# Kernel optimization log

Measured on AMD Instinct MI355X. Metric: run time of the kernel, lower is better.

Reference implementation:

```python
import jax, jax.numpy as jnp
import numpy as np

N_NODES = 100000
N_EDGES = 3200000
IN_DIM = 512
LATENT_DIM = 128


def spmm(row, col, vals, z, n):
    # sparse [n,n] @ z: out[r] = sum_e vals[e] * z[col[e]] for edges with row[e]==r
    msgs = vals[:, None] * z[col]  # [E, d]
    return jax.ops.segment_sum(msgs, row, num_segments=n)


def setup_inputs() -> dict:
    key = jax.random.key(0)
    k1, k2, k3, k4, k5, k6, k7 = jax.random.split(key, 7)
    x = jax.random.normal(k1, (N_NODES, IN_DIM), dtype=jnp.float32)
    # xavier-uniform-like init
    lim_e = float(np.sqrt(6.0 / (IN_DIM + LATENT_DIM)))
    W_enc = jax.random.uniform(k2, (IN_DIM, LATENT_DIM), minval=-lim_e, maxval=lim_e, dtype=jnp.float32)
    W_dec = jax.random.uniform(k3, (LATENT_DIM, IN_DIM), minval=-lim_e, maxval=lim_e, dtype=jnp.float32)
    row = jax.random.randint(k4, (N_EDGES,), 0, N_NODES, dtype=jnp.int32)
    col = jax.random.randint(k5, (N_EDGES,), 0, N_NODES, dtype=jnp.int32)
    vals = jax.random.uniform(k6, (N_EDGES,), dtype=jnp.float32)
    perm = jax.random.permutation(k7, N_NODES).astype(jnp.int32)
    return {"x": x, "W_enc": W_enc, "W_dec": W_dec, "vals": vals,
            "row": row, "col": col, "perm": perm}


def reference(x, W_enc, W_dec, vals, row, col, perm):
    n = x.shape[0]
    # encoder GCN: h = adj @ (x @ W_enc)
    h = spmm(row, col, vals, x @ W_enc, n)
    # decoder GCN: out = adj @ (h @ W_dec)
    out = spmm(row, col, vals, h @ W_dec, n)
    # corrupted view: row-permuted features through the encoder
    x_a = x[perm]
    h_a = spmm(row, col, vals, x_a @ W_enc, n)
    return (out, h, h_a)
```

## Files before the change

kernel.cpp:

```cpp
#include <hip/hip_runtime.h>
#include <hip/hip_bf16.h>


#define THREADS 256


__global__ void zero_i32(int* __restrict__ p, int n) {
    int i = blockIdx.x * blockDim.x + threadIdx.x;
    if (i < n) p[i] = 0;
}

__global__ void copy_i32(const int* __restrict__ src, int* __restrict__ dst, int n) {
    int i = blockIdx.x * blockDim.x + threadIdx.x;
    if (i < n) dst[i] = src[i];
}

__global__ void hist_rows(const int* __restrict__ row, int* __restrict__ cnt, int E) {
    for (int e = blockIdx.x * blockDim.x + threadIdx.x; e < E; e += gridDim.x * blockDim.x)
        atomicAdd(&cnt[row[e]], 1);
}

__global__ void scan_partial(const int* __restrict__ cnt, int* __restrict__ bsum, int n) {
    __shared__ int red[256];
    int t = threadIdx.x;
    int base = blockIdx.x * 1024 + t * 4;
    int s = 0;
#pragma unroll
    for (int i = 0; i < 4; ++i) {
        int idx = base + i;
        if (idx < n) s += cnt[idx];
    }
    red[t] = s;
    __syncthreads();
    for (int off = 128; off > 0; off >>= 1) {
        if (t < off) red[t] += red[t + off];
        __syncthreads();
    }
    if (t == 0) bsum[blockIdx.x] = red[0];
}

__global__ void scan_bsum(const int* __restrict__ bsum, int* __restrict__ bscan,
                          int nb, int* __restrict__ rowptr, int n, int E) {
    __shared__ int s[128];
    int t = threadIdx.x;
    int v = (t < nb) ? bsum[t] : 0;
    s[t] = v;
    __syncthreads();
    for (int off = 1; off < 128; off <<= 1) {
        int x = (t >= off) ? s[t - off] : 0;
        __syncthreads();
        s[t] += x;
        __syncthreads();
    }
    if (t < nb) bscan[t] = s[t] - v;
    if (t == 0) rowptr[n] = E;
}

__global__ void scan_final(const int* __restrict__ cnt, const int* __restrict__ bscan,
                           int* __restrict__ rowptr, int n) {
    __shared__ int tsum[256];
    int t = threadIdx.x;
    int base = blockIdx.x * 1024 + t * 4;
    int v[4];
#pragma unroll
    for (int i = 0; i < 4; ++i) {
        int idx = base + i;
        v[i] = (idx < n) ? cnt[idx] : 0;
    }
    int tot = v[0] + v[1] + v[2] + v[3];
    tsum[t] = tot;
    __syncthreads();
    for (int off = 1; off < 256; off <<= 1) {
        int x = (t >= off) ? tsum[t - off] : 0;
        __syncthreads();
        tsum[t] += x;
        __syncthreads();
    }
    int run = tsum[t] - tot + bscan[blockIdx.x];
#pragma unroll
    for (int i = 0; i < 4; ++i) {
        int idx = base + i;
        if (idx < n) rowptr[idx] = run;
        run += v[i];
    }
}

__global__ void scatter_edges(const int* __restrict__ row, const int* __restrict__ col,
                              const float* __restrict__ vals, int* __restrict__ cursor,
                              int* __restrict__ scol, float* __restrict__ sval, int E) {
    for (int e = blockIdx.x * blockDim.x + threadIdx.x; e < E; e += gridDim.x * blockDim.x) {
        int r = row[e];
        int p = atomicAdd(&cursor[r], 1);
        scol[p] = col[e];
        sval[p] = vals[e];
    }
}

__global__ __launch_bounds__(256) void gemm_f32(const float* __restrict__ A,
                                                const float* __restrict__ B,
                                                float* __restrict__ C,
                                                int M, int N, int K) {
    __shared__ float As[16][68];
    __shared__ float Bs[16][128];
    int t = threadIdx.x;
    int tr = t >> 5;
    int tc = t & 31;
    int rbase = blockIdx.x * 64;
    int cb = blockIdx.y * 128;

    float acc[8][4];
#pragma unroll
    for (int i = 0; i < 8; ++i)
#pragma unroll
        for (int j = 0; j < 4; ++j) acc[i][j] = 0.f;

    int arow = t >> 2;
    int akq = (t & 3) * 4;

    for (int kt = 0; kt < K; kt += 16) {
        float4 av = make_float4(0.f, 0.f, 0.f, 0.f);
        if (rbase + arow < M)
            av = *(const float4*)&A[(size_t)(rbase + arow) * K + kt + akq];
        As[akq + 0][arow] = av.x;
        As[akq + 1][arow] = av.y;
        As[akq + 2][arow] = av.z;
        As[akq + 3][arow] = av.w;
        {
            int s0 = t;
            int k0 = s0 >> 5, c0 = (s0 & 31) * 4;
            *(float4*)&Bs[k0][c0] = *(const float4*)&B[(size_t)(kt + k0) * N + cb + c0];
            int s1 = t + 256;
            int k1 = s1 >> 5, c1 = (s1 & 31) * 4;
            *(float4*)&Bs[k1][c1] = *(const float4*)&B[(size_t)(kt + k1) * N + cb + c1];
        }
        __syncthreads();
#pragma unroll
        for (int kk = 0; kk < 16; ++kk) {
            float4 a0 = *(const float4*)&As[kk][tr * 8];
            float4 a1 = *(const float4*)&As[kk][tr * 8 + 4];
            float4 b = *(const float4*)&Bs[kk][tc * 4];
            float a[8] = {a0.x, a0.y, a0.z, a0.w, a1.x, a1.y, a1.z, a1.w};
#pragma unroll
            for (int i = 0; i < 8; ++i) {
                acc[i][0] += a[i] * b.x;
                acc[i][1] += a[i] * b.y;
                acc[i][2] += a[i] * b.z;
                acc[i][3] += a[i] * b.w;
            }
        }
        __syncthreads();
    }
#pragma unroll
    for (int i = 0; i < 8; ++i) {
        int r = rbase + tr * 8 + i;
        if (r < M)
            *(float4*)&C[(size_t)r * N + cb + tc * 4] =
                make_float4(acc[i][0], acc[i][1], acc[i][2], acc[i][3]);
    }
}

__global__ __launch_bounds__(256) void spmm128(const int* __restrict__ rowptr,
                                               const int* __restrict__ scol,
                                               const float* __restrict__ sval,
                                               const float* __restrict__ z,
                                               float* __restrict__ out,
                                               const int* __restrict__ perm, int n) {
    int t = threadIdx.x;
    int r = blockIdx.x * 8 + (t >> 5);
    if (r >= n) return;
    int lane4 = (t & 31) * 4;
    int s = rowptr[r], e1 = rowptr[r + 1];
    float4 acc = make_float4(0.f, 0.f, 0.f, 0.f);
    for (int e = s; e < e1; ++e) {
        int c = scol[e];
        if (perm) c = perm[c];
        float v = sval[e];
        float4 zv = *(const float4*)&z[(size_t)c * 128 + lane4];
        acc.x += v * zv.x;
        acc.y += v * zv.y;
        acc.z += v * zv.z;
        acc.w += v * zv.w;
    }
    *(float4*)&out[(size_t)r * 128 + lane4] = acc;
}


extern "C" void kernel_launch(void* const* d_in, const int* in_sizes, int n_in,
                              void* d_out, int out_size, void* d_ws, size_t ws_size,
                              hipStream_t stream) {
    const float* x     = (const float*)d_in[0];
    const float* W_enc = (const float*)d_in[1];
    const float* W_dec = (const float*)d_in[2];
    const float* vals  = (const float*)d_in[3];
    const int*   row   = (const int*)d_in[4];
    const int*   col   = (const int*)d_in[5];
    const int*   perm  = (const int*)d_in[6];
    const int n = in_sizes[6];
    const int E = in_sizes[4];
    const int IN = 512, L = 128;

    float* out0  = (float*)d_out;
    float* outh  = out0 + (size_t)n * IN;
    float* outha = outh + (size_t)n * L;

    char* w = (char*)d_ws;
    auto alloc = [&](size_t bytes) -> char* {
        char* p = w;
        w += (bytes + 255) & ~(size_t)255;
        return p;
    };
    float* z1     = (float*)alloc((size_t)n * L * 4);
    float* g      = (float*)alloc((size_t)n * L * 4);
    int*   scol   = (int*)alloc((size_t)E * 4);
    float* sval   = (float*)alloc((size_t)E * 4);
    int*   rowptr = (int*)alloc((size_t)(n + 1) * 4);
    int*   cursor = (int*)alloc((size_t)n * 4);
    int*   cnt    = (int*)alloc((size_t)n * 4);
    int*   bsum   = (int*)alloc(128 * 4);
    int*   bscan  = (int*)alloc(128 * 4);

    const int nb = (n + 1023) / 1024;

    hipLaunchKernelGGL(zero_i32, dim3((n + 255) / 256), dim3(256), 0, stream, cnt, n);
    hipLaunchKernelGGL(hist_rows, dim3(2048), dim3(256), 0, stream, row, cnt, E);
    hipLaunchKernelGGL(scan_partial, dim3(nb), dim3(256), 0, stream, cnt, bsum, n);
    hipLaunchKernelGGL(scan_bsum, dim3(1), dim3(128), 0, stream, bsum, bscan, nb, rowptr, n, E);
    hipLaunchKernelGGL(scan_final, dim3(nb), dim3(256), 0, stream, cnt, bscan, rowptr, n);
    hipLaunchKernelGGL(copy_i32, dim3((n + 255) / 256), dim3(256), 0, stream, rowptr, cursor, n);
    hipLaunchKernelGGL(scatter_edges, dim3(2048), dim3(256), 0, stream,
                       row, col, vals, cursor, scol, sval, E);

    hipLaunchKernelGGL(gemm_f32, dim3((n + 63) / 64, 1), dim3(256), 0, stream,
                       x, W_enc, z1, n, L, IN);
    hipLaunchKernelGGL(spmm128, dim3((n + 7) / 8), dim3(256), 0, stream,
                       rowptr, scol, sval, z1, outh, (const int*)nullptr, n);
    hipLaunchKernelGGL(spmm128, dim3((n + 7) / 8), dim3(256), 0, stream,
                       rowptr, scol, sval, z1, outha, perm, n);
    hipLaunchKernelGGL(spmm128, dim3((n + 7) / 8), dim3(256), 0, stream,
                       rowptr, scol, sval, outh, g, (const int*)nullptr, n);
    hipLaunchKernelGGL(gemm_f32, dim3((n + 63) / 64, 4), dim3(256), 0, stream,
                       g, W_dec, out0, n, IN, L);
}
```

Measured before the change: 1.767 ms.

## Store SpMM operands in bf16, pack edges, fuse encoder and corrupted SpMMs

The encoder GEMM now writes z in bf16, and h is also stored as a bf16 copy for the decoder SpMM. This halves the bytes of the random gathers that dominate the SpMM kernels. Column and value are packed into one 8-byte edge record, and the h and h_a SpMMs are fused so each edge is read once with two gathers. Each row is handled by 16 lanes with 8 features per lane. The cost is bf16 rounding error in the intermediates, which may exceed the output tolerance.

Result: faster. 1.460 ms (-17.4%).

```diff
diff --git a/kernel.cpp b/kernel.cpp
--- a/kernel.cpp
+++ b/kernel.cpp
@@ -2,7 +2,15 @@
 #include <hip/hip_bf16.h>
 
 
-#define THREADS 256
+typedef unsigned int uint;
+typedef unsigned short ushort;
+
+__device__ inline ushort f2bf(float f) {
+    uint u = __float_as_uint(f);
+    return (ushort)((u + 0x7FFFu + ((u >> 16) & 1u)) >> 16);
+}
+__device__ inline float bflo(uint u) { return __uint_as_float(u << 16); }
+__device__ inline float bfhi(uint u) { return __uint_as_float(u & 0xFFFF0000u); }
 
 
 __global__ void zero_i32(int* __restrict__ p, int n) {
@@ -87,18 +95,18 @@
 
 __global__ void scatter_edges(const int* __restrict__ row, const int* __restrict__ col,
                               const float* __restrict__ vals, int* __restrict__ cursor,
-                              int* __restrict__ scol, float* __restrict__ sval, int E) {
+                              uint2* __restrict__ ep, int E) {
     for (int e = blockIdx.x * blockDim.x + threadIdx.x; e < E; e += gridDim.x * blockDim.x) {
         int r = row[e];
         int p = atomicAdd(&cursor[r], 1);
-        scol[p] = col[e];
-        sval[p] = vals[e];
+        ep[p] = make_uint2((uint)col[e], __float_as_uint(vals[e]));
     }
 }
 
 __global__ __launch_bounds__(256) void gemm_f32(const float* __restrict__ A,
                                                 const float* __restrict__ B,
-                                                float* __restrict__ C,
+                                                float* __restrict__ Cf,
+                                                ushort* __restrict__ Cb,
                                                 int M, int N, int K) {
     __shared__ float As[16][68];
     __shared__ float Bs[16][128];
@@ -153,35 +161,88 @@
 #pragma unroll
     for (int i = 0; i < 8; ++i) {
         int r = rbase + tr * 8 + i;
-        if (r < M)
-            *(float4*)&C[(size_t)r * N + cb + tc * 4] =
-                make_float4(acc[i][0], acc[i][1], acc[i][2], acc[i][3]);
-    }
-}
-
-__global__ __launch_bounds__(256) void spmm128(const int* __restrict__ rowptr,
-                                               const int* __restrict__ scol,
-                                               const float* __restrict__ sval,
-                                               const float* __restrict__ z,
-                                               float* __restrict__ out,
-                                               const int* __restrict__ perm, int n) {
-    int t = threadIdx.x;
-    int r = blockIdx.x * 8 + (t >> 5);
+        if (r < M) {
+            if (Cb) {
+                ushort4 o;
+                o.x = f2bf(acc[i][0]);
+                o.y = f2bf(acc[i][1]);
+                o.z = f2bf(acc[i][2]);
+                o.w = f2bf(acc[i][3]);
+                *(ushort4*)&Cb[(size_t)r * N + cb + tc * 4] = o;
+            } else {
+                *(float4*)&Cf[(size_t)r * N + cb + tc * 4] =
+                    make_float4(acc[i][0], acc[i][1], acc[i][2], acc[i][3]);
+            }
+        }
+    }
+}
+
+__global__ __launch_bounds__(256) void spmm_fused(const int* __restrict__ rowptr,
+                                                  const uint2* __restrict__ ep,
+                                                  const ushort* __restrict__ zb,
+                                                  const int* __restrict__ perm,
+                                                  float* __restrict__ outh,
+                                                  float* __restrict__ outha,
+                                                  ushort* __restrict__ hb, int n) {
+    int t = threadIdx.x;
+    int r = blockIdx.x * 16 + (t >> 4);
     if (r >= n) return;
-    int lane4 = (t & 31) * 4;
+    int lo = (t & 15) * 8;
     int s = rowptr[r], e1 = rowptr[r + 1];
-    float4 acc = make_float4(0.f, 0.f, 0.f, 0.f);
+    float ah[8] = {0, 0, 0, 0, 0, 0, 0, 0};
+    float aa[8] = {0, 0, 0, 0, 0, 0, 0, 0};
     for (int e = s; e < e1; ++e) {
-        int c = scol[e];
-        if (perm) c = perm[c];
-        float v = sval[e];
-        float4 zv = *(const float4*)&z[(size_t)c * 128 + lane4];
-        acc.x += v * zv.x;
-        acc.y += v * zv.y;
-        acc.z += v * zv.z;
-        acc.w += v * zv.w;
-    }
-    *(float4*)&out[(size_t)r * 128 + lane4] = acc;
+        uint2 ed = ep[e];
+        int c = (int)ed.x;
+        float v = __uint_as_float(ed.y);
+        int c2 = perm[c];
+        uint4 za = *(const uint4*)&zb[(size_t)c * 128 + lo];
+        uint4 zp = *(const uint4*)&zb[(size_t)c2 * 128 + lo];
+        ah[0] += v * bflo(za.x); ah[1] += v * bfhi(za.x);
+        ah[2] += v * bflo(za.y); ah[3] += v * bfhi(za.y);
+        ah[4] += v * bflo(za.z); ah[5] += v * bfhi(za.z);
+        ah[6] += v * bflo(za.w); ah[7] += v * bfhi(za.w);
+        aa[0] += v * bflo(zp.x); aa[1] += v * bfhi(zp.x);
+        aa[2] += v * bflo(zp.y); aa[3] += v * bfhi(zp.y);
+        aa[4] += v * bflo(zp.z); aa[5] += v * bfhi(zp.z);
+        aa[6] += v * bflo(zp.w); aa[7] += v * bfhi(zp.w);
+    }
+    size_t o = (size_t)r * 128 + lo;
+    *(float4*)&outh[o]     = make_float4(ah[0], ah[1], ah[2], ah[3]);
+    *(float4*)&outh[o + 4] = make_float4(ah[4], ah[5], ah[6], ah[7]);
+    *(float4*)&outha[o]     = make_float4(aa[0], aa[1], aa[2], aa[3]);
+    *(float4*)&outha[o + 4] = make_float4(aa[4], aa[5], aa[6], aa[7]);
+    uint4 hp;
+    hp.x = (uint)f2bf(ah[0]) | ((uint)f2bf(ah[1]) << 16);
+    hp.y = (uint)f2bf(ah[2]) | ((uint)f2bf(ah[3]) << 16);
+    hp.z = (uint)f2bf(ah[4]) | ((uint)f2bf(ah[5]) << 16);
+    hp.w = (uint)f2bf(ah[6]) | ((uint)f2bf(ah[7]) << 16);
+    *(uint4*)&hb[o] = hp;
+}
+
+__global__ __launch_bounds__(256) void spmm_single(const int* __restrict__ rowptr,
+                                                   const uint2* __restrict__ ep,
+                                                   const ushort* __restrict__ zb,
+                                                   float* __restrict__ out, int n) {
+    int t = threadIdx.x;
+    int r = blockIdx.x * 16 + (t >> 4);
+    if (r >= n) return;
+    int lo = (t & 15) * 8;
+    int s = rowptr[r], e1 = rowptr[r + 1];
+    float ah[8] = {0, 0, 0, 0, 0, 0, 0, 0};
+    for (int e = s; e < e1; ++e) {
+        uint2 ed = ep[e];
+        int c = (int)ed.x;
+        float v = __uint_as_float(ed.y);
+        uint4 za = *(const uint4*)&zb[(size_t)c * 128 + lo];
+        ah[0] += v * bflo(za.x); ah[1] += v * bfhi(za.x);
+        ah[2] += v * bflo(za.y); ah[3] += v * bfhi(za.y);
+        ah[4] += v * bflo(za.z); ah[5] += v * bfhi(za.z);
+        ah[6] += v * bflo(za.w); ah[7] += v * bfhi(za.w);
+    }
+    size_t o = (size_t)r * 128 + lo;
+    *(float4*)&out[o]     = make_float4(ah[0], ah[1], ah[2], ah[3]);
+    *(float4*)&out[o + 4] = make_float4(ah[4], ah[5], ah[6], ah[7]);
 }
 
 
@@ -209,10 +270,10 @@
         w += (bytes + 255) & ~(size_t)255;
         return p;
     };
-    float* z1     = (float*)alloc((size_t)n * L * 4);
-    float* g      = (float*)alloc((size_t)n * L * 4);
-    int*   scol   = (int*)alloc((size_t)E * 4);
-    float* sval   = (float*)alloc((size_t)E * 4);
+    ushort* z1b   = (ushort*)alloc((size_t)n * L * 2);
+    ushort* hb    = (ushort*)alloc((size_t)n * L * 2);
+    float*  g     = (float*)alloc((size_t)n * L * 4);
+    uint2*  ep    = (uint2*)alloc((size_t)E * 8);
     int*   rowptr = (int*)alloc((size_t)(n + 1) * 4);
     int*   cursor = (int*)alloc((size_t)n * 4);
     int*   cnt    = (int*)alloc((size_t)n * 4);
@@ -228,16 +289,14 @@
     hipLaunchKernelGGL(scan_final, dim3(nb), dim3(256), 0, stream, cnt, bscan, rowptr, n);
     hipLaunchKernelGGL(copy_i32, dim3((n + 255) / 256), dim3(256), 0, stream, rowptr, cursor, n);
     hipLaunchKernelGGL(scatter_edges, dim3(2048), dim3(256), 0, stream,
-                       row, col, vals, cursor, scol, sval, E);
+                       row, col, vals, cursor, ep, E);
 
     hipLaunchKernelGGL(gemm_f32, dim3((n + 63) / 64, 1), dim3(256), 0, stream,
-                       x, W_enc, z1, n, L, IN);
-    hipLaunchKernelGGL(spmm128, dim3((n + 7) / 8), dim3(256), 0, stream,
-                       rowptr, scol, sval, z1, outh, (const int*)nullptr, n);
-    hipLaunchKernelGGL(spmm128, dim3((n + 7) / 8), dim3(256), 0, stream,
-                       rowptr, scol, sval, z1, outha, perm, n);
-    hipLaunchKernelGGL(spmm128, dim3((n + 7) / 8), dim3(256), 0, stream,
-                       rowptr, scol, sval, outh, g, (const int*)nullptr, n);
+                       x, W_enc, (float*)nullptr, z1b, n, L, IN);
+    hipLaunchKernelGGL(spmm_fused, dim3((n + 15) / 16), dim3(256), 0, stream,
+                       rowptr, ep, z1b, perm, outh, outha, hb, n);
+    hipLaunchKernelGGL(spmm_single, dim3((n + 15) / 16), dim3(256), 0, stream,
+                       rowptr, ep, hb, g, n);
     hipLaunchKernelGGL(gemm_f32, dim3((n + 63) / 64, 4), dim3(256), 0, stream,
-                       g, W_dec, out0, n, IN, L);
-}
+                       g, W_dec, out0, (ushort*)nullptr, n, IN, L);
+}
```
